# Performance work log

Measured on AMD Instinct MI355X. Metric: run time of the kernel, lower is better.

## Reference

```python
import jax, jax.numpy as jnp
import numpy as np

N = 32768      # total nodes per batched graph
E = 262144     # edges per batched graph (avg in-degree 8)
B = 64         # number of graphs in the batch (for mean_nodes readout)
DIN = 20
H = 512
BN_EPS = 1e-5


def setup_inputs() -> dict:
    key = jax.random.key(0)
    ks = jax.random.split(key, 24)
    p = lambda k, shape: jax.random.normal(k, shape, jnp.float32) * 0.02
    inp = {
        "x1": jax.random.normal(ks[0], (N, DIN), jnp.float32),
        "x2": jax.random.normal(ks[1], (N, DIN), jnp.float32),
        "src1": jax.random.randint(ks[2], (E,), 0, N, jnp.int32),
        "dst1": jax.random.randint(ks[3], (E,), 0, N, jnp.int32),
        "src2": jax.random.randint(ks[4], (E,), 0, N, jnp.int32),
        "dst2": jax.random.randint(ks[5], (E,), 0, N, jnp.int32),
        "gids1": jnp.repeat(jnp.arange(B, dtype=jnp.int32), N // B),
        "gids2": jnp.repeat(jnp.arange(B, dtype=jnp.int32), N // B),
        # shared parameters (applied to both graphs, as in the torch module)
        "W_init": p(ks[6], (DIN, H)), "b_init": jnp.zeros((H,), jnp.float32),
        "W1": p(ks[7], (H, H)), "b1": jnp.zeros((H,), jnp.float32),
        "W2": p(ks[8], (H, H)), "b2": jnp.zeros((H,), jnp.float32),
        "gamma1": jnp.ones((H,), jnp.float32), "beta1": jnp.zeros((H,), jnp.float32),
        "gamma2": jnp.ones((H,), jnp.float32), "beta2": jnp.zeros((H,), jnp.float32),
        "Wfc": p(ks[9], (2 * H, 256)), "bfc": jnp.zeros((256,), jnp.float32),
        "Wfc2": p(ks[10], (256, 1)), "bfc2": jnp.zeros((1,), jnp.float32),
    }
    return inp


def _bn_relu(z, gamma, beta):
    # BatchNorm1d in training mode: biased batch stats over the node axis
    mu = jnp.mean(z, axis=0)
    var = jnp.var(z, axis=0)
    return jax.nn.relu(gamma * (z - mu) * jax.lax.rsqrt(var + BN_EPS) + beta)


def _gin_mean(h, src, dst, W, b):
    # DGL GINConv(apply=Linear, aggregator='mean', eps=0):
    # out = Linear(h + mean_{j in N_in(v)} h_j); isolated nodes get 0 agg.
    msg_sum = jax.ops.segment_sum(h[src], dst, num_segments=N)      # [N,H]
    deg = jax.ops.segment_sum(jnp.ones((src.shape[0],), h.dtype), dst, num_segments=N)
    agg = msg_sum / jnp.maximum(deg, 1.0)[:, None]
    return (h + agg) @ W + b


def _encode(x, src, dst, gids, W_init, b_init, W1, b1, W2, b2,
            gamma1, beta1, gamma2, beta2):
    h0 = x @ W_init + b_init
    h1 = _bn_relu(_gin_mean(h0, src, dst, W1, b1), gamma1, beta1)
    h2 = _bn_relu(_gin_mean(h1, src, dst, W2, b2), gamma2, beta2)
    # dgl.mean_nodes: per-graph mean over nodes
    s = jax.ops.segment_sum(h2, gids, num_segments=B)               # [B,H]
    cnt = jax.ops.segment_sum(jnp.ones((h2.shape[0],), h2.dtype), gids, num_segments=B)
    return s / jnp.maximum(cnt, 1.0)[:, None]


def reference(x1, x2, src1, dst1, src2, dst2, gids1, gids2,
              W_init, b_init, W1, b1, W2, b2,
              gamma1, beta1, gamma2, beta2, Wfc, bfc, Wfc2, bfc2):
    g1_emb = _encode(x1, src1, dst1, gids1, W_init, b_init, W1, b1, W2, b2,
                     gamma1, beta1, gamma2, beta2)
    g2_emb = _encode(x2, src2, dst2, gids2, W_init, b_init, W1, b1, W2, b2,
                     gamma1, beta1, gamma2, beta2)
    x = jnp.concatenate([g1_emb, g2_emb], axis=1)                   # [B,2H]
    x = jax.nn.relu(x @ Wfc + bfc)
    return jax.nn.sigmoid(x @ Wfc2 + bfc2)                          # [B,1]
```

## Files before the change

kernel.cpp:

```cpp
#include <hip/hip_runtime.h>
#include <hip/hip_bf16.h>
#include <cstdint>

#define NN 32768
#define EE 262144
#define MM 65536
#define HH 512
#define BB 64
#define DIN 20
#define BN_EPS 1e-5f

__device__ __forceinline__ float bflo(uint32_t w) { return __builtin_bit_cast(float, w << 16); }
__device__ __forceinline__ float bfhi(uint32_t w) { return __builtin_bit_cast(float, w & 0xffff0000u); }
__device__ __forceinline__ uint32_t f2bf_u(float f) {
  uint32_t u = __builtin_bit_cast(uint32_t, f);
  return (u + 0x7fffu + ((u >> 16) & 1u)) >> 16;
}
__device__ __forceinline__ uint32_t pack2(float lo, float hi) {
  return f2bf_u(lo) | (f2bf_u(hi) << 16);
}

typedef float f32x4 __attribute__((ext_vector_type(4)));
typedef float f32x2 __attribute__((ext_vector_type(2)));

__device__ __forceinline__ void gl2lds16(const void* g, void* l) {
  __builtin_amdgcn_global_load_lds(
      (const __attribute__((address_space(1))) void*)g,
      (__attribute__((address_space(3))) void*)l, 16, 0, 0);
}

__global__ void prep_deg_kernel(const int* __restrict__ dst1, const int* __restrict__ dst2,
                                int* __restrict__ deg_cnt,
                                const float* __restrict__ W2, uint32_t* __restrict__ Wt8,
                                const float* __restrict__ Wi, const float* __restrict__ bi,
                                const float* __restrict__ W1, float* __restrict__ Wf) {
  int bid = blockIdx.x;
  if (bid < 2048) {
    int e = bid * 256 + threadIdx.x;
    int g = e >> 18, le = e & 0x3ffff;
    int d = (g ? dst2 : dst1)[le];
    atomicAdd(&deg_cnt[g * NN + d], 1);
  } else if (bid < 2304) {
    int idx = (bid - 2048) * 256 + threadIdx.x;
    int n = idx >> 7, k4 = idx & 127;
    int k = k4 * 4;
    float w0 = W2[(size_t)k * HH + n];
    float w1 = W2[(size_t)(k + 1) * HH + n];
    float w2v = W2[(size_t)(k + 2) * HH + n];
    float w3 = W2[(size_t)(k + 3) * HH + n];
    uint32_t p = __builtin_amdgcn_cvt_pk_fp8_f32(w0, w1, 0u, false);
    p = __builtin_amdgcn_cvt_pk_fp8_f32(w2v, w3, p, true);
    Wt8[(size_t)n * 128 + k4] = p;
  } else {
    int idx = (bid - 2304) * 256 + threadIdx.x;
    if (idx >= 21 * 512) return;
    int k = idx >> 9, n = idx & 511;
    float s = 0.f;
    if (k < 20) {
      const float* wr = Wi + (size_t)k * HH;
      for (int j = 0; j < HH; j++) s = fmaf(wr[j], W1[(size_t)j * HH + n], s);
    } else {
      for (int j = 0; j < HH; j++) s = fmaf(bi[j], W1[(size_t)j * HH + n], s);
    }
    Wf[idx] = s;
  }
}

__global__ void scan_kernel(const int* __restrict__ deg_cnt, int* __restrict__ offsets,
                            int* __restrict__ cursor) {
  int g = blockIdx.x;
  const int* d = deg_cnt + g * NN;
  int* off = offsets + g * (NN + 1);
  int* cur = cursor + g * NN;
  int t = threadIdx.x;
  int base = t * 32;
  int loc[32]; int s = 0;
#pragma unroll
  for (int i = 0; i < 32; i++) { loc[i] = d[base + i]; s += loc[i]; }
  __shared__ int sm[1024];
  sm[t] = s; __syncthreads();
  for (int ofs = 1; ofs < 1024; ofs <<= 1) {
    int v = sm[t];
    int add = (t >= ofs) ? sm[t - ofs] : 0;
    __syncthreads();
    sm[t] = v + add;
    __syncthreads();
  }
  int run = (t == 0) ? 0 : sm[t - 1];
#pragma unroll
  for (int i = 0; i < 32; i++) { off[base + i] = run; cur[base + i] = run; run += loc[i]; }
  if (t == 1023) off[NN] = run;
}

__global__ void scatter_kernel(const int* __restrict__ src1, const int* __restrict__ dst1,
                               const int* __restrict__ src2, const int* __restrict__ dst2,
                               int* __restrict__ cursor, int* __restrict__ csr) {
  int e = blockIdx.x * 256 + threadIdx.x;
  int g = e >> 18, le = e & 0x3ffff;
  int d = (g ? dst2 : dst1)[le];
  int s = (g ? src2 : src1)[le];
  int pos = atomicAdd(&cursor[g * NN + d], 1);
  csr[g * EE + pos] = s;
}

__global__ __launch_bounds__(512) void z1_kernel(const float* __restrict__ x1,
                          const float* __restrict__ x2,
                          const int* __restrict__ csr, const int* __restrict__ offsets,
                          const float* __restrict__ Wf, const float* __restrict__ b1,
                          uint32_t* __restrict__ z8, float* __restrict__ pstat) {
  __shared__ float xas[128][21];
  __shared__ float sred[512][8];
  int t = threadIdx.x;
  int r0 = blockIdx.x * 128;
  int g = r0 >> 15;
  const float* xg = g ? x2 : x1;
  const int* off = offsets + g * (NN + 1);
  const int* cs = csr + g * EE;

  {
    int row = t >> 2;
    int q = t & 3;
    int n = (r0 + row) & (NN - 1);
    int e0 = off[n], e1 = off[n + 1];
    float4 a4[5] = {};
    for (int e = e0 + q; e < e1; e += 4) {
      const float4* xr = (const float4*)(xg + (size_t)cs[e] * DIN);
#pragma unroll
      for (int k = 0; k < 5; k++) {
        float4 v = xr[k];
        a4[k].x += v.x; a4[k].y += v.y; a4[k].z += v.z; a4[k].w += v.w;
      }
    }
#pragma unroll
    for (int k = 0; k < 5; k++) {
      a4[k].x += __shfl_xor(a4[k].x, 1); a4[k].y += __shfl_xor(a4[k].y, 1);
      a4[k].z += __shfl_xor(a4[k].z, 1); a4[k].w += __shfl_xor(a4[k].w, 1);
      a4[k].x += __shfl_xor(a4[k].x, 2); a4[k].y += __shfl_xor(a4[k].y, 2);
      a4[k].z += __shfl_xor(a4[k].z, 2); a4[k].w += __shfl_xor(a4[k].w, 2);
    }
    if (q == 0) {
      float inv = (e1 > e0) ? 1.f / (float)(e1 - e0) : 0.f;
      const float4* xs = (const float4*)(xg + (size_t)n * DIN);
#pragma unroll
      for (int k = 0; k < 5; k++) {
        float4 v = xs[k];
        xas[row][k * 4 + 0] = fmaf(a4[k].x, inv, v.x);
        xas[row][k * 4 + 1] = fmaf(a4[k].y, inv, v.y);
        xas[row][k * 4 + 2] = fmaf(a4[k].z, inv, v.z);
        xas[row][k * 4 + 3] = fmaf(a4[k].w, inv, v.w);
      }
    }
  }
  __syncthreads();

  int col0 = (t & 127) * 4;
  int rq = t >> 7;

  float w[DIN][4];
#pragma unroll
  for (int k = 0; k < DIN; k++) {
    float4 wv = *(const float4*)(Wf + (size_t)k * HH + col0);
    w[k][0] = wv.x; w[k][1] = wv.y; w[k][2] = wv.z; w[k][3] = wv.w;
  }
  float4 bvv = *(const float4*)(Wf + (size_t)DIN * HH + col0);
  float4 b1v = *(const float4*)(b1 + col0);

  float s4[4] = {0.f, 0.f, 0.f, 0.f}, q4[4] = {0.f, 0.f, 0.f, 0.f};
  for (int rr = 0; rr < 32; rr++) {
    int row = rr * 4 + rq;
    int grow = r0 + row;
    int n = grow & (NN - 1);
    float bf = (off[n + 1] - off[n] > 0) ? 2.f : 1.f;
    float a0 = fmaf(bvv.x, bf, b1v.x), a1 = fmaf(bvv.y, bf, b1v.y);
    float a2 = fmaf(bvv.z, bf, b1v.z), a3 = fmaf(bvv.w, bf, b1v.w);
#pragma unroll
    for (int k = 0; k < DIN; k++) {
      float xv = xas[row][k];
      a0 = fmaf(xv, w[k][0], a0);
      a1 = fmaf(xv, w[k][1], a1);
      a2 = fmaf(xv, w[k][2], a2);
      a3 = fmaf(xv, w[k][3], a3);
    }
    s4[0] += a0; q4[0] = fmaf(a0, a0, q4[0]);
    s4[1] += a1; q4[1] = fmaf(a1, a1, q4[1]);
    s4[2] += a2; q4[2] = fmaf(a2, a2, q4[2]);
    s4[3] += a3; q4[3] = fmaf(a3, a3, q4[3]);
    uint32_t p8 = __builtin_amdgcn_cvt_pk_fp8_f32(a0, a1, 0u, false);
    p8 = __builtin_amdgcn_cvt_pk_fp8_f32(a2, a3, p8, true);
    z8[(size_t)grow * 128 + (col0 >> 2)] = p8;
  }

#pragma unroll
  for (int k = 0; k < 4; k++) { sred[t][k] = s4[k]; sred[t][4 + k] = q4[k]; }
  __syncthreads();
  if (t < 128) {
    float* p = pstat + (size_t)blockIdx.x * 1024 + (size_t)col0 * 2;
#pragma unroll
    for (int k = 0; k < 4; k++) {
      p[k * 2 + 0] = sred[t][k] + sred[t + 128][k] + sred[t + 256][k] + sred[t + 384][k];
      p[k * 2 + 1] = sred[t][4 + k] + sred[t + 128][4 + k] + sred[t + 256][4 + k] + sred[t + 384][4 + k];
    }
  }
}

__global__ void reduce_stats(const float* __restrict__ pstat, const float* __restrict__ gamma,
                             const float* __restrict__ beta, float* __restrict__ scsh, int nsl) {
  int b = blockIdx.x;
  int g = b >> 4, cg = b & 15;
  int t = threadIdx.x;
  int c = cg * 32 + (t & 31);
  int s = t >> 5;
  int per = nsl >> 3;
  const float2* p = (const float2*)pstat + ((size_t)(g * nsl + s * per)) * 512 + c;
  float sum = 0.f, q = 0.f;
  for (int m = 0; m < per; m++) { float2 v = p[(size_t)m * 512]; sum += v.x; q += v.y; }
  __shared__ float ls[8][64];
  ls[s][(t & 31) * 2] = sum; ls[s][(t & 31) * 2 + 1] = q;
  __syncthreads();
  if (t < 32) {
    float S = 0.f, Q = 0.f;
#pragma unroll
    for (int k = 0; k < 8; k++) { S += ls[k][t * 2]; Q += ls[k][t * 2 + 1]; }
    int cc = cg * 32 + t;
    float mu = S * (1.f / (float)NN);
    float var = fmaxf(Q * (1.f / (float)NN) - mu * mu, 0.f);
    float sc = gamma[cc] * rsqrtf(var + BN_EPS);
    scsh[g * 1024 + cc * 2] = sc;
    scsh[g * 1024 + cc * 2 + 1] = beta[cc] - mu * sc;
  }
}

__device__ __forceinline__ void bn_acc8_fp8(uint2 v, const f32x2* sc2, const f32x2* sh2,
                                            f32x2* acc) {
  f32x2 f[4];
  f[0] = __builtin_amdgcn_cvt_pk_f32_fp8(v.x, false);
  f[1] = __builtin_amdgcn_cvt_pk_f32_fp8(v.x, true);
  f[2] = __builtin_amdgcn_cvt_pk_f32_fp8(v.y, false);
  f[3] = __builtin_amdgcn_cvt_pk_f32_fp8(v.y, true);
#pragma unroll
  for (int i = 0; i < 4; i++) {
    f32x2 y = f[i] * sc2[i] + sh2[i];
    y.x = fmaxf(y.x, 0.f); y.y = fmaxf(y.y, 0.f);
    acc[i] += y;
  }
}

__global__ __launch_bounds__(256) void aggbn_kernel(const uint32_t* __restrict__ z8,
                             uint32_t* __restrict__ u8,
                             const int* __restrict__ csr, const int* __restrict__ offsets,
                             const float* __restrict__ scsh) {
  int wid = (blockIdx.x * 256 + threadIdx.x) >> 6;
  int lane = threadIdx.x & 63;
  int g = wid >> 15, n = wid & (NN - 1);
  const int* off = offsets + g * (NN + 1);
  int e0 = off[n], e1 = off[n + 1];
  const int* cs = csr + g * EE;
  const uint32_t* base8 = z8 + (size_t)g * NN * 128 + lane * 2;

  uint2 hv8 = *(const uint2*)(base8 + (size_t)n * 128);

  const float4* ssp = (const float4*)(scsh + (size_t)g * HH * 2 + lane * 16);
  float4 ss0 = ssp[0], ss1 = ssp[1], ss2 = ssp[2], ss3 = ssp[3];
  f32x2 sc2[4], sh2[4];
  sc2[0] = f32x2{ss0.x, ss0.z}; sh2[0] = f32x2{ss0.y, ss0.w};
  sc2[1] = f32x2{ss1.x, ss1.z}; sh2[1] = f32x2{ss1.y, ss1.w};
  sc2[2] = f32x2{ss2.x, ss2.z}; sh2[2] = f32x2{ss2.y, ss2.w};
  sc2[3] = f32x2{ss3.x, ss3.z}; sh2[3] = f32x2{ss3.y, ss3.w};
  f32x2 acc2[4] = {f32x2{0.f, 0.f}, f32x2{0.f, 0.f}, f32x2{0.f, 0.f}, f32x2{0.f, 0.f}};

  int e = e0;
  int rem = e1 - e0;
  int s0 = 0, s1 = 0, s2 = 0, s3 = 0;
  if (rem >= 4) { s0 = cs[e]; s1 = cs[e + 1]; s2 = cs[e + 2]; s3 = cs[e + 3]; }
  while (rem >= 4) {
    uint2 v0 = *(const uint2*)(base8 + (size_t)s0 * 128);
    uint2 v1 = *(const uint2*)(base8 + (size_t)s1 * 128);
    uint2 v2 = *(const uint2*)(base8 + (size_t)s2 * 128);
    uint2 v3 = *(const uint2*)(base8 + (size_t)s3 * 128);
    e += 4; rem -= 4;
    if (rem >= 4) { s0 = cs[e]; s1 = cs[e + 1]; s2 = cs[e + 2]; s3 = cs[e + 3]; }
    bn_acc8_fp8(v0, sc2, sh2, acc2);
    bn_acc8_fp8(v1, sc2, sh2, acc2);
    bn_acc8_fp8(v2, sc2, sh2, acc2);
    bn_acc8_fp8(v3, sc2, sh2, acc2);
  }
  for (; rem > 0; rem--, e++) {
    int s = cs[e];
    uint2 v = *(const uint2*)(base8 + (size_t)s * 128);
    bn_acc8_fp8(v, sc2, sh2, acc2);
  }

  float inv = (e1 > e0) ? 1.f / (float)(e1 - e0) : 0.f;
  f32x2 h01 = __builtin_amdgcn_cvt_pk_f32_fp8(hv8.x, false);
  f32x2 h23 = __builtin_amdgcn_cvt_pk_f32_fp8(hv8.x, true);
  f32x2 h45 = __builtin_amdgcn_cvt_pk_f32_fp8(hv8.y, false);
  f32x2 h67 = __builtin_amdgcn_cvt_pk_f32_fp8(hv8.y, true);
  f32x2 hs[4] = {h01, h23, h45, h67};
  float o[8];
#pragma unroll
  for (int i = 0; i < 4; i++) {
    f32x2 y = hs[i] * sc2[i] + sh2[i];
    o[2 * i]     = fmaxf(y.x, 0.f) + acc2[i].x * inv;
    o[2 * i + 1] = fmaxf(y.y, 0.f) + acc2[i].y * inv;
  }
  uint32_t q0 = __builtin_amdgcn_cvt_pk_fp8_f32(o[0], o[1], 0u, false);
  q0 = __builtin_amdgcn_cvt_pk_fp8_f32(o[2], o[3], q0, true);
  uint32_t q1 = __builtin_amdgcn_cvt_pk_fp8_f32(o[4], o[5], 0u, false);
  q1 = __builtin_amdgcn_cvt_pk_fp8_f32(o[6], o[7], q1, true);
  uint2 ov; ov.x = q0; ov.y = q1;
  *(uint2*)(u8 + (size_t)wid * 128 + lane * 2) = ov;
}

__global__ __launch_bounds__(512) void gemm_kernel(const uint8_t* __restrict__ A8,
                                                   const uint8_t* __restrict__ Bt8,
                                                   const float* __restrict__ bias,
                                                   uint8_t* __restrict__ Z2,
                                                   float* __restrict__ pstat) {
  __shared__ __align__(16) char lds[49152];
  uint8_t* sA = (uint8_t*)lds;
  uint8_t* sB = (uint8_t*)lds + 32768;
  const int tid = threadIdx.x;
  const int wave = tid >> 6;
  const int lane = tid & 63;
  const int bid = blockIdx.x;
  const int xcd = bid & 7;
  const int l = bid >> 3;
  const int nb = l & 3;
  const int mb = xcd * 32 + (l >> 2);
  const int m0 = mb * 256;
  const int n0 = nb * 128;
  const int fm = lane & 15;
  const int quad = lane >> 4;
  const int wr = wave >> 1, wc = wave & 1;

  const int sr = lane >> 3;
  const int slot = lane & 7;

  f32x4 acc[4][4] = {};
  for (int k0 = 0; k0 < HH; k0 += 128) {
    __syncthreads();
#pragma unroll
    for (int t = 0; t < 4; t++) {
      int R = t * 64 + wave * 8 + sr;
      int ksw = (slot ^ (R & 7)) * 16;
      gl2lds16(A8 + (size_t)(m0 + R) * HH + k0 + ksw, sA + R * 128 + slot * 16);
      if (t < 2)
        gl2lds16(Bt8 + (size_t)(n0 + R) * HH + k0 + ksw, sB + R * 128 + slot * 16);
    }
    __syncthreads();
#pragma unroll
    for (int s2 = 0; s2 < 4; s2++) {
      const int k8 = s2 * 4 + quad;
      const int k16 = k8 >> 1;
      const int h8 = (k8 & 1) * 8;
      long a[4], b[4];
#pragma unroll
      for (int i = 0; i < 4; i++) {
        int r = wr * 64 + i * 16 + fm;
        a[i] = *(const long*)(sA + r * 128 + ((k16 ^ (r & 7)) * 16) + h8);
      }
#pragma unroll
      for (int j = 0; j < 4; j++) {
        int r = wc * 64 + j * 16 + fm;
        b[j] = *(const long*)(sB + r * 128 + ((k16 ^ (r & 7)) * 16) + h8);
      }
#pragma unroll
      for (int i = 0; i < 4; i++)
#pragma unroll
        for (int j = 0; j < 4; j++)
          acc[i][j] = __builtin_amdgcn_mfma_f32_16x16x32_fp8_fp8(a[i], b[j], acc[i][j], 0, 0, 0);
    }
  }

  float bj4[4];
#pragma unroll
  for (int j = 0; j < 4; j++) bj4[j] = bias[n0 + wc * 64 + j * 16 + fm];

  __syncthreads();
  float* ls = (float*)lds;
  if (tid < 256) ls[tid] = 0.f;
  __syncthreads();
#pragma unroll
  for (int j = 0; j < 4; j++) {
    int colloc = wc * 64 + j * 16 + fm;
    float sj = 0.f, qj = 0.f;
#pragma unroll
    for (int i = 0; i < 4; i++)
#pragma unroll
      for (int r = 0; r < 4; r++) {
        float f = acc[i][j][r] + bj4[j];
        sj += f; qj = fmaf(f, f, qj);
      }
    atomicAdd(&ls[colloc * 2], sj);
    atomicAdd(&ls[colloc * 2 + 1], qj);
  }
  __syncthreads();
  if (tid < 128) {
    float* p = pstat + (size_t)mb * 1024 + (size_t)(n0 + tid) * 2;
    p[0] = ls[tid * 2];
    p[1] = ls[tid * 2 + 1];
  }
  __syncthreads();

  uint16_t* sC = (uint16_t*)lds;
#pragma unroll
  for (int h = 0; h < 2; h++) {
    if ((wr >> 1) == h) {
      int lrb = (wr & 1) * 64;
#pragma unroll
      for (int j = 0; j < 4; j++) {
        int col = wc * 64 + j * 16 + fm;
#pragma unroll
        for (int i = 0; i < 4; i++) {
          int rb = lrb + i * 16 + quad * 4;
#pragma unroll
          for (int r = 0; r < 4; r++)
            sC[(rb + r) * 136 + col] = (uint16_t)f2bf_u(acc[i][j][r] + bj4[j]);
        }
      }
    }
    __syncthreads();
    int orow = tid >> 3;
    int oc16 = (tid & 7) * 16;
#pragma unroll
    for (int r2 = 0; r2 < 2; r2++) {
      int row = r2 * 64 + orow;
      uint4 va = *(const uint4*)(sC + row * 136 + oc16);
      uint4 vb = *(const uint4*)(sC + row * 136 + oc16 + 8);
      uint32_t wv[8] = {va.x, va.y, va.z, va.w, vb.x, vb.y, vb.z, vb.w};
      uint4 o8;
      uint32_t* op = (uint32_t*)&o8;
#pragma unroll
      for (int q = 0; q < 4; q++) {
        uint32_t p8 = __builtin_amdgcn_cvt_pk_fp8_f32(bflo(wv[2 * q]), bfhi(wv[2 * q]), 0u, false);
        p8 = __builtin_amdgcn_cvt_pk_fp8_f32(bflo(wv[2 * q + 1]), bfhi(wv[2 * q + 1]), p8, true);
        op[q] = p8;
      }
      *(uint4*)(Z2 + (size_t)(m0 + h * 128 + row) * HH + n0 + oc16) = o8;
    }
    __syncthreads();
  }
}

__global__ void bn2_readout(const uint32_t* __restrict__ z2, const float* __restrict__ scsh,
                            const int* __restrict__ gids1, const int* __restrict__ gids2,
                            float* __restrict__ readout, float* __restrict__ cnt) {
  int blk = blockIdx.x;
  int r0 = blk * 128;
  int g = r0 >> 15;
  int lr = r0 & (NN - 1);
  int gid = (g ? gids2 : gids1)[lr];
  int t = threadIdx.x;
  int cg = t & 127, rh = t >> 7;
  const float* ss = scsh + (size_t)g * HH * 2 + cg * 8;
  float4 s0 = *(const float4*)ss, s1 = *(const float4*)(ss + 4);
  f32x2 sc01 = f32x2{s0.x, s0.z}, sh01 = f32x2{s0.y, s0.w};
  f32x2 sc23 = f32x2{s1.x, s1.z}, sh23 = f32x2{s1.y, s1.w};
  const uint32_t* p = z2 + (size_t)(r0 + rh * 64) * 128 + cg;
  f32x2 a01 = f32x2{0.f, 0.f}, a23 = f32x2{0.f, 0.f};
  for (int r = 0; r < 64; r++) {
    uint32_t w = p[(size_t)r * 128];
    f32x2 f01 = __builtin_amdgcn_cvt_pk_f32_fp8(w, false);
    f32x2 f23 = __builtin_amdgcn_cvt_pk_f32_fp8(w, true);
    f32x2 y0 = f01 * sc01 + sh01;
    f32x2 y1 = f23 * sc23 + sh23;
    y0.x = fmaxf(y0.x, 0.f); y0.y = fmaxf(y0.y, 0.f);
    y1.x = fmaxf(y1.x, 0.f); y1.y = fmaxf(y1.y, 0.f);
    a01 += y0; a23 += y1;
  }
  __shared__ float sr2[128][4];
  if (rh) { sr2[cg][0] = a01.x; sr2[cg][1] = a01.y; sr2[cg][2] = a23.x; sr2[cg][3] = a23.y; }
  __syncthreads();
  if (!rh) {
    float* ro = readout + ((size_t)g * BB + gid) * HH;
    atomicAdd(&ro[cg * 4 + 0], a01.x + sr2[cg][0]);
    atomicAdd(&ro[cg * 4 + 1], a01.y + sr2[cg][1]);
    atomicAdd(&ro[cg * 4 + 2], a23.x + sr2[cg][2]);
    atomicAdd(&ro[cg * 4 + 3], a23.y + sr2[cg][3]);
  }
  if (t == 0) atomicAdd(&cnt[g * BB + gid], 128.f);
}

__global__ void final_kernel(const float* __restrict__ readout, const float* __restrict__ cnt,
                             const float* __restrict__ Wfc, const float* __restrict__ bfc,
                             const float* __restrict__ Wfc2, const float* __restrict__ bfc2,
                             float* __restrict__ out) {
  __shared__ float x[1024];
  __shared__ float red[256];
  int b = blockIdx.x, t = threadIdx.x;
  for (int i = t; i < 1024; i += 256) {
    int g = i >> 9, c = i & 511;
    float cc = cnt[g * BB + b];
    x[i] = readout[((size_t)g * BB + b) * HH + c] / fmaxf(cc, 1.f);
  }
  __syncthreads();
  float a0 = 0.f, a1 = 0.f, a2 = 0.f, a3 = 0.f;
  for (int i = 0; i < 1024; i += 4) {
    a0 = fmaf(x[i],     Wfc[(size_t)i * 256 + t],       a0);
    a1 = fmaf(x[i + 1], Wfc[(size_t)(i + 1) * 256 + t], a1);
    a2 = fmaf(x[i + 2], Wfc[(size_t)(i + 2) * 256 + t], a2);
    a3 = fmaf(x[i + 3], Wfc[(size_t)(i + 3) * 256 + t], a3);
  }
  float acc = bfc[t] + ((a0 + a1) + (a2 + a3));
  red[t] = fmaxf(acc, 0.f) * Wfc2[t];
  __syncthreads();
  for (int s = 128; s > 0; s >>= 1) {
    if (t < s) red[t] += red[t + s];
    __syncthreads();
  }
  if (t == 0) out[b] = 1.f / (1.f + expf(-(red[0] + bfc2[0])));
}

extern "C" void kernel_launch(void* const* d_in, const int* in_sizes, int n_in,
                              void* d_out, int out_size, void* d_ws, size_t ws_size,
                              hipStream_t stream) {
  const float* x1 = (const float*)d_in[0];
  const float* x2 = (const float*)d_in[1];
  const int* src1 = (const int*)d_in[2];
  const int* dst1 = (const int*)d_in[3];
  const int* src2 = (const int*)d_in[4];
  const int* dst2 = (const int*)d_in[5];
  const int* gids1 = (const int*)d_in[6];
  const int* gids2 = (const int*)d_in[7];
  const float* Wi = (const float*)d_in[8];
  const float* bi = (const float*)d_in[9];
  const float* W1 = (const float*)d_in[10];
  const float* b1 = (const float*)d_in[11];
  const float* W2 = (const float*)d_in[12];
  const float* b2 = (const float*)d_in[13];
  const float* gamma1 = (const float*)d_in[14];
  const float* beta1 = (const float*)d_in[15];
  const float* gamma2 = (const float*)d_in[16];
  const float* beta2 = (const float*)d_in[17];
  const float* Wfc = (const float*)d_in[18];
  const float* bfc = (const float*)d_in[19];
  const float* Wfc2 = (const float*)d_in[20];
  const float* bfc2 = (const float*)d_in[21];
  float* out = (float*)d_out;

  size_t off = 0;
  auto alloc = [&](size_t bytes) -> void* {
    void* p = (char*)d_ws + off;
    off += (bytes + 255) & ~(size_t)255;
    return p;
  };
  uint32_t* z8 = (uint32_t*)alloc((size_t)MM * HH);
  uint32_t* u8 = (uint32_t*)alloc((size_t)MM * HH);
  uint8_t* z2o = (uint8_t*)alloc((size_t)MM * HH);
  uint32_t* Wt8 = (uint32_t*)alloc((size_t)HH * HH);
  float* Wf = (float*)alloc((size_t)(DIN + 1) * HH * 4);
  int* csr = (int*)alloc((size_t)2 * EE * 4);
  int* offsets = (int*)alloc((size_t)2 * (NN + 1) * 4);
  int* cursor = (int*)alloc((size_t)2 * NN * 4);
  float* pbuf1 = (float*)alloc((size_t)512 * 512 * 2 * 4);
  float* pbuf2 = (float*)alloc((size_t)256 * 512 * 2 * 4);
  size_t zero_begin = off;
  int* deg_cnt = (int*)alloc((size_t)2 * NN * 4);
  float* readout = (float*)alloc((size_t)2 * BB * HH * 4);
  float* cnt = (float*)alloc((size_t)2 * BB * 4);
  size_t zero_end = off;
  float* scsh1 = (float*)alloc((size_t)2 * HH * 2 * 4);
  float* scsh2 = (float*)alloc((size_t)2 * HH * 2 * 4);
  (void)ws_size; (void)in_sizes; (void)n_in; (void)out_size;

  hipMemsetAsync((char*)d_ws + zero_begin, 0, zero_end - zero_begin, stream);

  prep_deg_kernel<<<2304 + 42, 256, 0, stream>>>(dst1, dst2, deg_cnt, W2, Wt8, Wi, bi, W1, Wf);
  scan_kernel<<<2, 1024, 0, stream>>>(deg_cnt, offsets, cursor);
  scatter_kernel<<<2048, 256, 0, stream>>>(src1, dst1, src2, dst2, cursor, csr);

  z1_kernel<<<MM / 128, 512, 0, stream>>>(x1, x2, csr, offsets, Wf, b1, z8, pbuf1);
  reduce_stats<<<32, 256, 0, stream>>>(pbuf1, gamma1, beta1, scsh1, 256);

  aggbn_kernel<<<MM / 4, 256, 0, stream>>>(z8, u8, csr, offsets, scsh1);
  gemm_kernel<<<1024, 512, 0, stream>>>((const uint8_t*)u8, (const uint8_t*)Wt8, b2, z2o, pbuf2);
  reduce_stats<<<32, 256, 0, stream>>>(pbuf2, gamma2, beta2, scsh2, 128);
  bn2_readout<<<512, 256, 0, stream>>>((const uint32_t*)z2o, scsh2, gids1, gids2, readout, cnt);

  final_kernel<<<BB, 256, 0, stream>>>(readout, cnt, Wfc, bfc, Wfc2, bfc2, out);
}
```

Measured before the change: 381.9 us.

## Shrink second-layer FP8 GEMM tile to 128x128 with 256 threads and wider LDS reads

The second-layer FP8 GEMM now uses 128x128 output tiles computed by 4 waves instead of 256x128 tiles with 8 waves. The grid doubles to 2048 blocks and the per-block partial-stat buffer and reduce count grow to match. LDS use drops, so more blocks can be resident per CU. Fragment loads become 16-byte reads that feed two MFMAs each. The epilogue now writes the whole tile to LDS in a single pass with a narrower row pitch. The cost is more blocks, more reloads of B tiles, and twice as many partial statistics to reduce.

```diff
diff --git a/kernel.cpp b/kernel.cpp
--- a/kernel.cpp
+++ b/kernel.cpp
@@ -22,6 +22,7 @@
 
 typedef float f32x4 __attribute__((ext_vector_type(4)));
 typedef float f32x2 __attribute__((ext_vector_type(2)));
+typedef long longx2 __attribute__((ext_vector_type(2)));
 
 __device__ __forceinline__ void gl2lds16(const void* g, void* l) {
   __builtin_amdgcn_global_load_lds(
@@ -311,14 +312,14 @@
   *(uint2*)(u8 + (size_t)wid * 128 + lane * 2) = ov;
 }
 
-__global__ __launch_bounds__(512) void gemm_kernel(const uint8_t* __restrict__ A8,
+__global__ __launch_bounds__(256) void gemm_kernel(const uint8_t* __restrict__ A8,
                                                    const uint8_t* __restrict__ Bt8,
                                                    const float* __restrict__ bias,
                                                    uint8_t* __restrict__ Z2,
                                                    float* __restrict__ pstat) {
-  __shared__ __align__(16) char lds[49152];
+  __shared__ __align__(16) char lds[33792];
   uint8_t* sA = (uint8_t*)lds;
-  uint8_t* sB = (uint8_t*)lds + 32768;
+  uint8_t* sB = (uint8_t*)lds + 16384;
   const int tid = threadIdx.x;
   const int wave = tid >> 6;
   const int lane = tid & 63;
@@ -326,8 +327,8 @@
   const int xcd = bid & 7;
   const int l = bid >> 3;
   const int nb = l & 3;
-  const int mb = xcd * 32 + (l >> 2);
-  const int m0 = mb * 256;
+  const int mb = xcd * 64 + (l >> 2);
+  const int m0 = mb * 128;
   const int n0 = nb * 128;
   const int fm = lane & 15;
   const int quad = lane >> 4;
@@ -341,34 +342,33 @@
     __syncthreads();
 #pragma unroll
     for (int t = 0; t < 4; t++) {
-      int R = t * 64 + wave * 8 + sr;
+      int R = t * 32 + wave * 8 + sr;
       int ksw = (slot ^ (R & 7)) * 16;
       gl2lds16(A8 + (size_t)(m0 + R) * HH + k0 + ksw, sA + R * 128 + slot * 16);
-      if (t < 2)
-        gl2lds16(Bt8 + (size_t)(n0 + R) * HH + k0 + ksw, sB + R * 128 + slot * 16);
+      gl2lds16(Bt8 + (size_t)(n0 + R) * HH + k0 + ksw, sB + R * 128 + slot * 16);
     }
     __syncthreads();
 #pragma unroll
-    for (int s2 = 0; s2 < 4; s2++) {
-      const int k8 = s2 * 4 + quad;
-      const int k16 = k8 >> 1;
-      const int h8 = (k8 & 1) * 8;
-      long a[4], b[4];
+    for (int s2 = 0; s2 < 2; s2++) {
+      const int k16 = s2 * 4 + quad;
+      longx2 a[4], b[4];
 #pragma unroll
       for (int i = 0; i < 4; i++) {
         int r = wr * 64 + i * 16 + fm;
-        a[i] = *(const long*)(sA + r * 128 + ((k16 ^ (r & 7)) * 16) + h8);
+        a[i] = *(const longx2*)(sA + r * 128 + ((k16 ^ (r & 7)) * 16));
       }
 #pragma unroll
       for (int j = 0; j < 4; j++) {
         int r = wc * 64 + j * 16 + fm;
-        b[j] = *(const long*)(sB + r * 128 + ((k16 ^ (r & 7)) * 16) + h8);
+        b[j] = *(const longx2*)(sB + r * 128 + ((k16 ^ (r & 7)) * 16));
       }
 #pragma unroll
       for (int i = 0; i < 4; i++)
 #pragma unroll
-        for (int j = 0; j < 4; j++)
-          acc[i][j] = __builtin_amdgcn_mfma_f32_16x16x32_fp8_fp8(a[i], b[j], acc[i][j], 0, 0, 0);
+        for (int j = 0; j < 4; j++) {
+          acc[i][j] = __builtin_amdgcn_mfma_f32_16x16x32_fp8_fp8(a[i][0], b[j][0], acc[i][j], 0, 0, 0);
+          acc[i][j] = __builtin_amdgcn_mfma_f32_16x16x32_fp8_fp8(a[i][1], b[j][1], acc[i][j], 0, 0, 0);
+        }
     }
   }
 
@@ -404,41 +404,33 @@
 
   uint16_t* sC = (uint16_t*)lds;
 #pragma unroll
-  for (int h = 0; h < 2; h++) {
-    if ((wr >> 1) == h) {
-      int lrb = (wr & 1) * 64;
-#pragma unroll
-      for (int j = 0; j < 4; j++) {
-        int col = wc * 64 + j * 16 + fm;
-#pragma unroll
-        for (int i = 0; i < 4; i++) {
-          int rb = lrb + i * 16 + quad * 4;
-#pragma unroll
-          for (int r = 0; r < 4; r++)
-            sC[(rb + r) * 136 + col] = (uint16_t)f2bf_u(acc[i][j][r] + bj4[j]);
-        }
-      }
-    }
-    __syncthreads();
-    int orow = tid >> 3;
+  for (int j = 0; j < 4; j++) {
+    int col = wc * 64 + j * 16 + fm;
+#pragma unroll
+    for (int i = 0; i < 4; i++) {
+      int rb = wr * 64 + i * 16 + quad * 4;
+#pragma unroll
+      for (int r = 0; r < 4; r++)
+        sC[(rb + r) * 132 + col] = (uint16_t)f2bf_u(acc[i][j][r] + bj4[j]);
+    }
+  }
+  __syncthreads();
+#pragma unroll
+  for (int r2 = 0; r2 < 4; r2++) {
+    int row = r2 * 32 + (tid >> 3);
     int oc16 = (tid & 7) * 16;
-#pragma unroll
-    for (int r2 = 0; r2 < 2; r2++) {
-      int row = r2 * 64 + orow;
-      uint4 va = *(const uint4*)(sC + row * 136 + oc16);
-      uint4 vb = *(const uint4*)(sC + row * 136 + oc16 + 8);
-      uint32_t wv[8] = {va.x, va.y, va.z, va.w, vb.x, vb.y, vb.z, vb.w};
-      uint4 o8;
-      uint32_t* op = (uint32_t*)&o8;
-#pragma unroll
-      for (int q = 0; q < 4; q++) {
-        uint32_t p8 = __builtin_amdgcn_cvt_pk_fp8_f32(bflo(wv[2 * q]), bfhi(wv[2 * q]), 0u, false);
-        p8 = __builtin_amdgcn_cvt_pk_fp8_f32(bflo(wv[2 * q + 1]), bfhi(wv[2 * q + 1]), p8, true);
-        op[q] = p8;
-      }
-      *(uint4*)(Z2 + (size_t)(m0 + h * 128 + row) * HH + n0 + oc16) = o8;
-    }
-    __syncthreads();
+    uint4 va = *(const uint4*)(sC + row * 132 + oc16);
+    uint4 vb = *(const uint4*)(sC + row * 132 + oc16 + 8);
+    uint32_t wv[8] = {va.x, va.y, va.z, va.w, vb.x, vb.y, vb.z, vb.w};
+    uint4 o8;
+    uint32_t* op = (uint32_t*)&o8;
+#pragma unroll
+    for (int q = 0; q < 4; q++) {
+      uint32_t p8 = __builtin_amdgcn_cvt_pk_fp8_f32(bflo(wv[2 * q]), bfhi(wv[2 * q]), 0u, false);
+      p8 = __builtin_amdgcn_cvt_pk_fp8_f32(bflo(wv[2 * q + 1]), bfhi(wv[2 * q + 1]), p8, true);
+      op[q] = p8;
+    }
+    *(uint4*)(Z2 + (size_t)(m0 + row) * HH + n0 + oc16) = o8;
   }
 }
 
@@ -553,7 +545,7 @@
   int* offsets = (int*)alloc((size_t)2 * (NN + 1) * 4);
   int* cursor = (int*)alloc((size_t)2 * NN * 4);
   float* pbuf1 = (float*)alloc((size_t)512 * 512 * 2 * 4);
-  float* pbuf2 = (float*)alloc((size_t)256 * 512 * 2 * 4);
+  float* pbuf2 = (float*)alloc((size_t)512 * 512 * 2 * 4);
   size_t zero_begin = off;
   int* deg_cnt = (int*)alloc((size_t)2 * NN * 4);
   float* readout = (float*)alloc((size_t)2 * BB * HH * 4);
@@ -573,8 +565,8 @@
   reduce_stats<<<32, 256, 0, stream>>>(pbuf1, gamma1, beta1, scsh1, 256);
 
   aggbn_kernel<<<MM / 4, 256, 0, stream>>>(z8, u8, csr, offsets, scsh1);
-  gemm_kernel<<<1024, 512, 0, stream>>>((const uint8_t*)u8, (const uint8_t*)Wt8, b2, z2o, pbuf2);
-  reduce_stats<<<32, 256, 0, stream>>>(pbuf2, gamma2, beta2, scsh2, 128);
+  gemm_kernel<<<2048, 256, 0, stream>>>((const uint8_t*)u8, (const uint8_t*)Wt8, b2, z2o, pbuf2);
+  reduce_stats<<<32, 256, 0, stream>>>(pbuf2, gamma2, beta2, scsh2, 256);
   bn2_readout<<<512, 256, 0, stream>>>((const uint32_t*)z2o, scsh2, gids1, gids2, readout, cnt);
 
   final_kernel<<<BB, 256, 0, stream>>>(readout, cnt, Wfc, bfc, Wfc2, bfc2, out);
```

New measurement: 374.8 us (median of 2 runs). No clear change (-1.9%).
